# Kernel tuning notes

Measured on AMD Instinct MI355X. Metric: run time of the kernel, lower is better.

## Reference

```python
import jax, jax.numpy as jnp
import numpy as np

N_NODES = 50000
EPS = 1e-7      # GENConv message epsilon
BN_EPS = 1e-5   # BatchNorm1d eps
N_AGGR = 2


def setup_inputs() -> dict:
    key = jax.random.key(0)
    ks = jax.random.split(key, 8)
    C = 64
    E = 800000
    x = jax.random.normal(ks[0], (N_NODES, C), dtype=jnp.float32)
    edge_index = jax.random.randint(ks[1], (2, E), 0, N_NODES, dtype=jnp.int64)
    # per-GENConv MLP params, stacked over the N_AGGR layers
    W1 = jax.random.normal(ks[2], (N_AGGR, C, 2 * C), dtype=jnp.float32) * (1.0 / np.sqrt(C))
    b1 = jnp.zeros((N_AGGR, 2 * C), dtype=jnp.float32)
    gamma = jnp.ones((N_AGGR, 2 * C), dtype=jnp.float32)
    beta = jnp.zeros((N_AGGR, 2 * C), dtype=jnp.float32)
    W2 = jax.random.normal(ks[3], (N_AGGR, 2 * C, C), dtype=jnp.float32) * (1.0 / np.sqrt(2 * C))
    b2 = jnp.zeros((N_AGGR, C), dtype=jnp.float32)
    t = jnp.ones((N_AGGR,), dtype=jnp.float32)  # learnable softmax temperature
    return {"x": x, "edge_index": edge_index, "W1": W1, "b1": b1,
            "gamma": gamma, "beta": beta, "W2": W2, "b2": b2, "t": t}


def _gen_conv(x, src, dst, W1_l, b1_l, gamma_l, beta_l, W2_l, b2_l, t_l):
    # message: relu(x_j) + eps  (edge_attr is None)
    m = jax.nn.relu(x[src]) + EPS                      # [E, C]
    # softmax aggregation over edges grouped by destination node
    logits = m * t_l                                   # [E, C]
    seg_max = jax.ops.segment_max(logits, dst, num_segments=N_NODES)  # [N, C]
    ex = jnp.exp(logits - seg_max[dst])                # [E, C]
    den = jax.ops.segment_sum(ex, dst, num_segments=N_NODES)          # [N, C]
    alpha = ex / (den[dst] + 1e-16)                    # [E, C]
    aggr = jax.ops.segment_sum(m * alpha, dst, num_segments=N_NODES)  # [N, C]
    # residual then MLP: Linear(C,2C) -> BatchNorm1d (train-mode stats) -> ReLU -> Linear(2C,C)
    h = aggr + x
    h = h @ W1_l + b1_l                                # [N, 2C]
    mean = h.mean(axis=0)
    var = h.var(axis=0)                                # biased variance (torch BN)
    h = (h - mean) / jnp.sqrt(var + BN_EPS) * gamma_l + beta_l
    h = jax.nn.relu(h)
    h = h @ W2_l + b2_l                                # [N, C]
    return h


def reference(x, edge_index, W1, b1, gamma, beta, W2, b2, t):
    src = edge_index[0]
    dst = edge_index[1]
    for l in range(N_AGGR):
        x = _gen_conv(x, src, dst, W1[l], b1[l], gamma[l], beta[l], W2[l], b2[l], t[l])
        x = jax.nn.relu(x)
        # dropout in eval mode == identity
    return x
```

## Files before the change

kernel.cpp:

```cpp
#include <hip/hip_runtime.h>
#include <math.h>

#define NN 50000
#define EPSM 1e-7f
#define BN_EPS 1e-5f
#define NBK 391
#define LOG2E 1.44269504088896340736f

#define BN_REP 32
#define MM_REP 8

#if defined(__has_builtin)
#if __has_builtin(__builtin_amdgcn_exp2f)
#define HAVE_EXP2_BUILTIN 1
#endif
#endif
__device__ __forceinline__ float fast_exp2(float v){
#ifdef HAVE_EXP2_BUILTIN
  return __builtin_amdgcn_exp2f(v);
#else
  return exp2f(v);
#endif
}


__global__ __launch_bounds__(256) void bucket_hist_kernel(
    const int* __restrict__ dst, int* __restrict__ bhist, int E,
    unsigned* __restrict__ mm0, float* __restrict__ bn0){
  __shared__ int h[NBK];
  int t = threadIdx.x;
  if (blockIdx.x == 0){
    for (int i = t; i < MM_REP * 128; i += 256)
      mm0[i] = ((i & 127) < 64) ? 0x7F7FFFFFu : 0u;
    for (int i = t; i < BN_REP * 256; i += 256) bn0[i] = 0.f;
  }
  for (int i = t; i < NBK; i += 256) h[i] = 0;
  __syncthreads();
  int e0 = blockIdx.x * 4096;
  int cnt = min(4096, E - e0);
  for (int i = t; i < cnt; i += 256) atomicAdd(&h[dst[e0 + i] >> 7], 1);
  __syncthreads();
  for (int i = t; i < NBK; i += 256) if (h[i]) atomicAdd(&bhist[i], h[i]);
}

__global__ void bucket_scan_kernel(const int* __restrict__ bhist,
                                   int* __restrict__ bbase, int* __restrict__ gcur){
  int lane = threadIdx.x;
  int loc[7]; int s = 0;
#pragma unroll
  for (int k = 0; k < 7; ++k){
    int i = lane * 7 + k;
    int v = (i < NBK) ? bhist[i] : 0;
    loc[k] = s; s += v;
  }
  int sc = s;
#pragma unroll
  for (int o = 1; o < 64; o <<= 1){
    int n = __shfl_up(sc, o);
    if (lane >= o) sc += n;
  }
  int exc = sc - s;
#pragma unroll
  for (int k = 0; k < 7; ++k){
    int i = lane * 7 + k;
    if (i < NBK){ bbase[i] = exc + loc[k]; gcur[i] = exc + loc[k]; }
    else if (i == NBK) bbase[i] = exc + loc[k];
  }
}

__global__ __launch_bounds__(256) void bucket_scatter_kernel(
    const int* __restrict__ src, const int* __restrict__ dst,
    int* __restrict__ gcur, unsigned* __restrict__ packed_g, int E){
  __shared__ int hist[NBK], offs[NBK], gb[NBK], curk[NBK];
  __shared__ unsigned stage[4096];
  __shared__ int gpos[4096];
  int t = threadIdx.x;
  for (int i = t; i < NBK; i += 256) hist[i] = 0;
  __syncthreads();
  int e0 = blockIdx.x * 4096;
  int cnt = min(4096, E - e0);
  unsigned pk[16]; int bk[16];
  int nmine = 0;
  for (int i = t; i < cnt; i += 256){
    int d = dst[e0 + i], s = src[e0 + i];
    pk[nmine] = ((unsigned)d << 16) | (unsigned)s;
    bk[nmine] = d >> 7;
    atomicAdd(&hist[bk[nmine]], 1);
    ++nmine;
  }
  __syncthreads();
  if (t < 64){
    int loc[7]; int s = 0;
#pragma unroll
    for (int k = 0; k < 7; ++k){
      int i = t * 7 + k;
      int v = (i < NBK) ? hist[i] : 0;
      loc[k] = s; s += v;
    }
    int sc = s;
#pragma unroll
    for (int o = 1; o < 64; o <<= 1){
      int n = __shfl_up(sc, o);
      if (t >= o) sc += n;
    }
    int exc = sc - s;
#pragma unroll
    for (int k = 0; k < 7; ++k){
      int i = t * 7 + k;
      if (i < NBK) offs[i] = exc + loc[k];
    }
  }
  __syncthreads();
  for (int i = t; i < NBK; i += 256){
    int h = hist[i];
    gb[i] = h ? atomicAdd(&gcur[i], h) : 0;
    curk[i] = offs[i];
  }
  __syncthreads();
  for (int k = 0; k < nmine; ++k){
    int b = bk[k];
    int p = atomicAdd(&curk[b], 1);
    stage[p] = pk[k];
    gpos[p] = gb[b] + (p - offs[b]);
  }
  __syncthreads();
  for (int j = t; j < cnt; j += 256) packed_g[gpos[j]] = stage[j];
}

__global__ __launch_bounds__(256) void bucket_place_kernel(
    const unsigned* __restrict__ packed_g, const int* __restrict__ bbase,
    int* __restrict__ start_g, int* __restrict__ end_g,
    unsigned short* __restrict__ srcs_g, int N){
  __shared__ int deg[128], off[128], cur[128];
  __shared__ int sstage[4096];
  int b = blockIdx.x, t = threadIdx.x;
  int beg = bbase[b], cnt = bbase[b + 1] - beg;
  if (t < 128) deg[t] = 0;
  __syncthreads();
  for (int j = t; j < cnt; j += 256)
    atomicAdd(&deg[(packed_g[beg + j] >> 16) & 127], 1);
  __syncthreads();
  if (t < 64){
    int i0 = t * 2;
    int v0 = deg[i0], v1 = deg[i0 + 1];
    int s = v0 + v1;
    int sc = s;
#pragma unroll
    for (int o = 1; o < 64; o <<= 1){
      int n = __shfl_up(sc, o);
      if (t >= o) sc += n;
    }
    int exc = sc - s;
    off[i0] = exc; off[i0 + 1] = exc + v0;
  }
  __syncthreads();
  int node0 = b * 128;
  if (t < 128){
    int node = node0 + t;
    if (node < N){
      start_g[node] = beg + off[t];
      end_g[node] = beg + off[t] + deg[t];
    }
    cur[t] = off[t];
  }
  __syncthreads();
  if (cnt <= 4096){
    for (int j = t; j < cnt; j += 256){
      unsigned p = packed_g[beg + j];
      int lp = atomicAdd(&cur[(p >> 16) & 127], 1);
      sstage[lp] = (int)(p & 0xFFFFu);
    }
    __syncthreads();
    for (int j = t; j < cnt; j += 256)
      srcs_g[beg + j] = (unsigned short)sstage[j];
  } else {
    for (int j = t; j < cnt; j += 256){
      unsigned p = packed_g[beg + j];
      int lp = atomicAdd(&cur[(p >> 16) & 127], 1);
      srcs_g[beg + lp] = (unsigned short)(p & 0xFFFFu);
    }
  }
}


__global__ __launch_bounds__(256) void colminmax_kernel(
    const float* __restrict__ x, unsigned* __restrict__ mm,
    unsigned short* __restrict__ mh, int N){
  __shared__ unsigned smn[256], smx[256];
  int c = threadIdx.x & 63;
  int slot = blockIdx.x * 4 + (threadIdx.x >> 6);
  float mx = 0.f, mn = 1e30f;
  for (int r = slot; r < N; r += 256 * 4){
    float m = fmaxf(x[r * 64 + c], 0.f) + EPSM;
    unsigned u = __float_as_uint(m);
    u += 0x7FFFu + ((u >> 16) & 1u);
    unsigned short us = (unsigned short)(u >> 16);
    mh[r * 64 + c] = us;
    float mb = __uint_as_float(((unsigned)us) << 16);
    mx = fmaxf(mx, mb);
    mn = fminf(mn, mb);
  }
  smn[threadIdx.x] = __float_as_uint(mn);
  smx[threadIdx.x] = __float_as_uint(mx);
  __syncthreads();
  if (threadIdx.x < 64){
    int rep = (blockIdx.x & (MM_REP - 1)) * 128;
    unsigned a = smn[c], b = smn[c + 64], d = smn[c + 128], e = smn[c + 192];
    atomicMin(&mm[rep + c], min(min(a, b), min(d, e)));
    a = smx[c]; b = smx[c + 64]; d = smx[c + 128]; e = smx[c + 192];
    atomicMax(&mm[rep + 64 + c], max(max(a, b), max(d, e)));
  }
}


__global__ __launch_bounds__(256) void aggregate_kernel(
    const float* __restrict__ x, const uint2* __restrict__ mh2,
    const int* __restrict__ start, const int* __restrict__ segend,
    const unsigned short* __restrict__ srcs, const float* __restrict__ tptr,
    int layer, const unsigned* __restrict__ mm, float* __restrict__ h0, int N){
  __shared__ float4 Bs4[16];
  int t = threadIdx.x;
  float t2 = tptr[layer] * LOG2E;
  if (t < 64){
    unsigned mn = 0x7F7FFFFFu, mx = 0u;
#pragma unroll
    for (int r = 0; r < MM_REP; ++r){
      mn = min(mn, mm[r * 128 + t]);
      mx = max(mx, mm[r * 128 + 64 + t]);
    }
    ((float*)Bs4)[t] = fmaxf(t2 * __uint_as_float(mx), t2 * __uint_as_float(mn));
  }
  __syncthreads();
  int node = blockIdx.x * 4 + (t >> 6);
  if (node >= N) return;
  int lane = t & 63;
  int slot = lane >> 4, cp = lane & 15;
  float4 B = Bs4[cp];
  int beg = start[node], end = segend[node];
  float d0 = 0.f, d1 = 0.f, d2 = 0.f, d3 = 0.f;
  float n0 = 0.f, n1 = 0.f, n2 = 0.f, n3 = 0.f;
  int e = beg;
  for (; e + 7 < end; e += 8){
    int sA = srcs[e + slot];
    int sB = srcs[e + 4 + slot];
    uint2 uA = mh2[sA * 16 + cp];
    uint2 uB = mh2[sB * 16 + cp];
    float a0 = __uint_as_float(uA.x << 16), a1 = __uint_as_float(uA.x & 0xFFFF0000u);
    float a2 = __uint_as_float(uA.y << 16), a3 = __uint_as_float(uA.y & 0xFFFF0000u);
    float b0 = __uint_as_float(uB.x << 16), b1 = __uint_as_float(uB.x & 0xFFFF0000u);
    float b2 = __uint_as_float(uB.y << 16), b3 = __uint_as_float(uB.y & 0xFFFF0000u);
    float pA0 = fast_exp2(fmaf(a0, t2, -B.x)), pA1 = fast_exp2(fmaf(a1, t2, -B.y));
    float pA2 = fast_exp2(fmaf(a2, t2, -B.z)), pA3 = fast_exp2(fmaf(a3, t2, -B.w));
    float pB0 = fast_exp2(fmaf(b0, t2, -B.x)), pB1 = fast_exp2(fmaf(b1, t2, -B.y));
    float pB2 = fast_exp2(fmaf(b2, t2, -B.z)), pB3 = fast_exp2(fmaf(b3, t2, -B.w));
    d0 += pA0 + pB0; n0 += a0 * pA0 + b0 * pB0;
    d1 += pA1 + pB1; n1 += a1 * pA1 + b1 * pB1;
    d2 += pA2 + pB2; n2 += a2 * pA2 + b2 * pB2;
    d3 += pA3 + pB3; n3 += a3 * pA3 + b3 * pB3;
  }
  for (; e + slot < end; e += 4){
    int s = srcs[e + slot];
    uint2 u = mh2[s * 16 + cp];
    float a0 = __uint_as_float(u.x << 16), a1 = __uint_as_float(u.x & 0xFFFF0000u);
    float a2 = __uint_as_float(u.y << 16), a3 = __uint_as_float(u.y & 0xFFFF0000u);
    float p0 = fast_exp2(fmaf(a0, t2, -B.x)), p1 = fast_exp2(fmaf(a1, t2, -B.y));
    float p2 = fast_exp2(fmaf(a2, t2, -B.z)), p3 = fast_exp2(fmaf(a3, t2, -B.w));
    d0 += p0; n0 += a0 * p0;  d1 += p1; n1 += a1 * p1;
    d2 += p2; n2 += a2 * p2;  d3 += p3; n3 += a3 * p3;
  }
  d0 += __shfl_xor(d0, 16); d1 += __shfl_xor(d1, 16);
  d2 += __shfl_xor(d2, 16); d3 += __shfl_xor(d3, 16);
  n0 += __shfl_xor(n0, 16); n1 += __shfl_xor(n1, 16);
  n2 += __shfl_xor(n2, 16); n3 += __shfl_xor(n3, 16);
  d0 += __shfl_xor(d0, 32); d1 += __shfl_xor(d1, 32);
  d2 += __shfl_xor(d2, 32); d3 += __shfl_xor(d3, 32);
  n0 += __shfl_xor(n0, 32); n1 += __shfl_xor(n1, 32);
  n2 += __shfl_xor(n2, 32); n3 += __shfl_xor(n3, 32);
  if (slot == 0){
    float4 xv = ((const float4*)x)[node * 16 + cp];
    float4 o;
    o.x = n0 / (d0 + 1e-16f) + xv.x;
    o.y = n1 / (d1 + 1e-16f) + xv.y;
    o.z = n2 / (d2 + 1e-16f) + xv.z;
    o.w = n3 / (d3 + 1e-16f) + xv.w;
    ((float4*)h0)[node * 16 + cp] = o;
  }
}


__global__ __launch_bounds__(256) void gemm1_kernel(
    const float* __restrict__ h0, const float* __restrict__ W1,
    const float* __restrict__ b1, float* __restrict__ h1,
    float* __restrict__ bn, int N,
    unsigned* __restrict__ mm_next, float* __restrict__ bn_next){
  __shared__ float a_lds[64 * 68];
  int t = threadIdx.x;
  if (mm_next != 0 && blockIdx.x == 0){
    for (int i = t; i < MM_REP * 128; i += 256)
      mm_next[i] = ((i & 127) < 64) ? 0x7F7FFFFFu : 0u;
    for (int i = t; i < BN_REP * 256; i += 256) bn_next[i] = 0.f;
  }
  int row0 = blockIdx.x * 64;
#pragma unroll
  for (int i = 0; i < 4; ++i){
    int li = t + 256 * i;
    int r = li >> 4, q = li & 15;
    int gr = row0 + r;
    float4 v = make_float4(0.f, 0.f, 0.f, 0.f);
    if (gr < N) v = ((const float4*)h0)[gr * 16 + q];
    *(float4*)&a_lds[r * 68 + q * 4] = v;
  }
  __syncthreads();
  int tc = t & 31, tr = t >> 5;
  float4 bias = ((const float4*)b1)[tc];
  float acc[8][4];
#pragma unroll
  for (int r = 0; r < 8; ++r){
    acc[r][0] = bias.x; acc[r][1] = bias.y; acc[r][2] = bias.z; acc[r][3] = bias.w;
  }
  const float4* wg = (const float4*)W1;
#pragma unroll 2
  for (int k = 0; k < 64; k += 4){
    float4 w0 = wg[(k + 0) * 32 + tc];
    float4 w1 = wg[(k + 1) * 32 + tc];
    float4 w2 = wg[(k + 2) * 32 + tc];
    float4 w3 = wg[(k + 3) * 32 + tc];
#pragma unroll
    for (int r = 0; r < 8; ++r){
      float4 a = *(const float4*)&a_lds[(tr * 8 + r) * 68 + k];
      acc[r][0] += a.x * w0.x + a.y * w1.x + a.z * w2.x + a.w * w3.x;
      acc[r][1] += a.x * w0.y + a.y * w1.y + a.z * w2.y + a.w * w3.y;
      acc[r][2] += a.x * w0.z + a.y * w1.z + a.z * w2.z + a.w * w3.z;
      acc[r][3] += a.x * w0.w + a.y * w1.w + a.z * w2.w + a.w * w3.w;
    }
  }
  float s[4] = {0.f, 0.f, 0.f, 0.f}, s2[4] = {0.f, 0.f, 0.f, 0.f};
#pragma unroll
  for (int r = 0; r < 8; ++r){
    int gr = row0 + tr * 8 + r;
    if (gr < N){
      *(float4*)&h1[gr * 128 + tc * 4] =
          make_float4(acc[r][0], acc[r][1], acc[r][2], acc[r][3]);
#pragma unroll
      for (int j = 0; j < 4; ++j){ s[j] += acc[r][j]; s2[j] += acc[r][j] * acc[r][j]; }
    }
  }
  __syncthreads();
  float* red = a_lds;
  if (t < 256){ red[t] = 0.f; }
  __syncthreads();
#pragma unroll
  for (int j = 0; j < 4; ++j){
    atomicAdd(&red[tc * 4 + j], s[j]);
    atomicAdd(&red[128 + tc * 4 + j], s2[j]);
  }
  __syncthreads();
  if (t < 256) atomicAdd(&bn[(blockIdx.x & (BN_REP - 1)) * 256 + t], red[t]);
}

__global__ __launch_bounds__(256) void gemm2_kernel(
    const float* __restrict__ h1, const float* __restrict__ bn,
    const float* __restrict__ gamma, const float* __restrict__ beta, int layer,
    const float* __restrict__ W2, const float* __restrict__ b2,
    float* __restrict__ xout, int N,
    unsigned* __restrict__ mm_next, unsigned short* __restrict__ mh_next){
  __shared__ float a_lds[64 * 132];
  __shared__ float ss[256];
  __shared__ unsigned smn[64], smx[64];
  int t = threadIdx.x;
  if (t < 128){
    float s = 0.f, s2 = 0.f;
#pragma unroll
    for (int r = 0; r < BN_REP; ++r){
      s  += bn[r * 256 + t];
      s2 += bn[r * 256 + 128 + t];
    }
    float mean = s * (1.f / (float)N);
    float var = s2 * (1.f / (float)N) - mean * mean;
    var = fmaxf(var, 0.f);
    float sc = gamma[layer * 128 + t] / sqrtf(var + BN_EPS);
    ss[t] = sc;
    ss[128 + t] = beta[layer * 128 + t] - mean * sc;
  }
  if (t < 64){ smn[t] = 0x7F7FFFFFu; smx[t] = 0u; }
  __syncthreads();
  int row0 = blockIdx.x * 64;
#pragma unroll
  for (int i = 0; i < 8; ++i){
    int li = t + 256 * i;
    int r = li >> 5, q = li & 31;
    int gr = row0 + r;
    float4 v = make_float4(0.f, 0.f, 0.f, 0.f);
    if (gr < N) v = ((const float4*)h1)[gr * 32 + q];
    float4 sc = *(const float4*)&ss[q * 4];
    float4 sh = *(const float4*)&ss[128 + q * 4];
    v.x = fmaxf(v.x * sc.x + sh.x, 0.f);
    v.y = fmaxf(v.y * sc.y + sh.y, 0.f);
    v.z = fmaxf(v.z * sc.z + sh.z, 0.f);
    v.w = fmaxf(v.w * sc.w + sh.w, 0.f);
    *(float4*)&a_lds[r * 132 + q * 4] = v;
  }
  __syncthreads();
  int tc = t & 15, tr = t >> 4;
  float4 bias = ((const float4*)b2)[tc];
  float acc[4][4];
#pragma unroll
  for (int r = 0; r < 4; ++r){
    acc[r][0] = bias.x; acc[r][1] = bias.y; acc[r][2] = bias.z; acc[r][3] = bias.w;
  }
  const float4* wg = (const float4*)W2;
#pragma unroll 2
  for (int k = 0; k < 128; k += 4){
    float4 w0 = wg[(k + 0) * 16 + tc];
    float4 w1 = wg[(k + 1) * 16 + tc];
    float4 w2 = wg[(k + 2) * 16 + tc];
    float4 w3 = wg[(k + 3) * 16 + tc];
#pragma unroll
    for (int r = 0; r < 4; ++r){
      float4 a = *(const float4*)&a_lds[(tr * 4 + r) * 132 + k];
      acc[r][0] += a.x * w0.x + a.y * w1.x + a.z * w2.x + a.w * w3.x;
      acc[r][1] += a.x * w0.y + a.y * w1.y + a.z * w2.y + a.w * w3.y;
      acc[r][2] += a.x * w0.z + a.y * w1.z + a.z * w2.z + a.w * w3.z;
      acc[r][3] += a.x * w0.w + a.y * w1.w + a.z * w2.w + a.w * w3.w;
    }
  }
  unsigned mnv[4] = {0x7F7FFFFFu, 0x7F7FFFFFu, 0x7F7FFFFFu, 0x7F7FFFFFu};
  unsigned mxv[4] = {0u, 0u, 0u, 0u};
#pragma unroll
  for (int r = 0; r < 4; ++r){
    int gr = row0 + tr * 4 + r;
    if (gr < N){
      float o0 = fmaxf(acc[r][0], 0.f), o1 = fmaxf(acc[r][1], 0.f);
      float o2 = fmaxf(acc[r][2], 0.f), o3 = fmaxf(acc[r][3], 0.f);
      *(float4*)&xout[gr * 64 + tc * 4] = make_float4(o0, o1, o2, o3);
      if (mh_next != 0){
        unsigned us[4];
        float ov[4] = {o0, o1, o2, o3};
#pragma unroll
        for (int j = 0; j < 4; ++j){
          unsigned u = __float_as_uint(ov[j] + EPSM);
          u += 0x7FFFu + ((u >> 16) & 1u);
          us[j] = u >> 16;
          unsigned fb = us[j] << 16;
          mnv[j] = min(mnv[j], fb);
          mxv[j] = max(mxv[j], fb);
        }
        ((uint2*)mh_next)[gr * 16 + tc] =
            make_uint2(us[0] | (us[1] << 16), us[2] | (us[3] << 16));
      }
    }
  }
  if (mh_next != 0){
    __syncthreads();
#pragma unroll
    for (int j = 0; j < 4; ++j){
      atomicMin(&smn[tc * 4 + j], mnv[j]);
      atomicMax(&smx[tc * 4 + j], mxv[j]);
    }
    __syncthreads();
    if (t < 64){
      int rep = (blockIdx.x & (MM_REP - 1)) * 128;
      atomicMin(&mm_next[rep + t], smn[t]);
      atomicMax(&mm_next[rep + 64 + t], smx[t]);
    }
  }
}

extern "C" void kernel_launch(void* const* d_in, const int* in_sizes, int n_in,
                              void* d_out, int out_size, void* d_ws, size_t ws_size,
                              hipStream_t stream) {
  const float* x0    = (const float*)d_in[0];
  const int*   ei    = (const int*)d_in[1];
  const float* W1    = (const float*)d_in[2];
  const float* b1    = (const float*)d_in[3];
  const float* gamma = (const float*)d_in[4];
  const float* beta  = (const float*)d_in[5];
  const float* W2    = (const float*)d_in[6];
  const float* b2    = (const float*)d_in[7];
  const float* tptr  = (const float*)d_in[8];

  const int N = NN;
  const int E = in_sizes[1] / 2;
  const int* src = ei;
  const int* dst = ei + E;

  float* ws  = (float*)d_ws;
  float* h0  = ws;
  float* h1  = h0 + N * 64;
  float* bn0 = h1 + N * 128;
  float* bn1 = bn0 + BN_REP * 256;
  unsigned* mm0 = (unsigned*)(bn1 + BN_REP * 256);
  unsigned* mm1 = mm0 + MM_REP * 128;
  unsigned short* mh = (unsigned short*)(mm1 + MM_REP * 128);
  int* bhist = (int*)(mh + N * 64);
  int* bbase = bhist + NBK;
  int* gcur  = bbase + NBK + 1;
  int* start = gcur + NBK;
  int* segend = start + N;
  unsigned* packed = (unsigned*)(segend + N);
  unsigned short* srcs = (unsigned short*)(packed + E);

  float* out = (float*)d_out;

  const int row_blocks = (N + 63) / 64;
  const int chunk_blocks = (E + 4095) / 4096;
  const int agg_blocks = (N + 3) / 4;

  hipMemsetAsync(bhist, 0, NBK * sizeof(int), stream);
  bucket_hist_kernel<<<chunk_blocks, 256, 0, stream>>>(dst, bhist, E, mm0, bn0);
  bucket_scan_kernel<<<1, 64, 0, stream>>>(bhist, bbase, gcur);
  bucket_scatter_kernel<<<chunk_blocks, 256, 0, stream>>>(src, dst, gcur, packed, E);
  bucket_place_kernel<<<NBK, 256, 0, stream>>>(packed, bbase, start, segend, srcs, N);

  colminmax_kernel<<<256, 256, 0, stream>>>(x0, mm0, mh, N);
  aggregate_kernel<<<agg_blocks, 256, 0, stream>>>(x0, (const uint2*)mh, start,
                                                   segend, srcs, tptr, 0, mm0, h0, N);
  gemm1_kernel<<<row_blocks, 256, 0, stream>>>(h0, W1, b1, h1, bn0, N, mm1, bn1);
  gemm2_kernel<<<row_blocks, 256, 0, stream>>>(h1, bn0, gamma, beta, 0, W2, b2,
                                               out, N, mm1, mh);
  aggregate_kernel<<<agg_blocks, 256, 0, stream>>>(out, (const uint2*)mh, start,
                                                   segend, srcs, tptr, 1, mm1, h0, N);
  gemm1_kernel<<<row_blocks, 256, 0, stream>>>(h0, W1 + 8192, b1 + 128, h1, bn1, N,
                                               (unsigned*)0, (float*)0);
  gemm2_kernel<<<row_blocks, 256, 0, stream>>>(h1, bn1, gamma, beta, 1, W2 + 8192,
                                               b2 + 64, out, N,
                                               (unsigned*)0, (unsigned short*)0);
}
```

Before: 300.9 us.

## Derive BatchNorm stats from input second moments and fuse both GEMMs

Instead of materializing the 128-wide hidden activation h1 to compute BatchNorm statistics, a moments kernel computes the 64x64 Gram matrix and column sums of the GEMM input. A single-block stats kernel then projects them through W1 to get the mean and variance of h1. A fused MLP kernel recomputes GEMM1, applies BN+ReLU in registers/LDS, and runs GEMM2, which removes the write and re-read of the 50000x128 h1 buffer. This adds a serial single-block reduction over 196 partials, redundant GEMM1 work, and a possible loss of precision from computing variance via E[x^2]-mean^2 on the projected moments.

New measurement: 433.6 us. 1.44x slower.

```diff
diff --git a/kernel.cpp b/kernel.cpp
--- a/kernel.cpp
+++ b/kernel.cpp
@@ -6,9 +6,9 @@
 #define BN_EPS 1e-5f
 #define NBK 391
 #define LOG2E 1.44269504088896340736f
-
-#define BN_REP 32
 #define MM_REP 8
+#define MOM_BLOCKS 196
+#define MOM_STRIDE 4352
 
 #if defined(__has_builtin)
 #if __has_builtin(__builtin_amdgcn_exp2f)
@@ -26,13 +26,12 @@
 
 __global__ __launch_bounds__(256) void bucket_hist_kernel(
     const int* __restrict__ dst, int* __restrict__ bhist, int E,
-    unsigned* __restrict__ mm0, float* __restrict__ bn0){
+    unsigned* __restrict__ mm0){
   __shared__ int h[NBK];
   int t = threadIdx.x;
   if (blockIdx.x == 0){
-    for (int i = t; i < MM_REP * 128; i += 256)
+    for (int i = t; i < 2 * MM_REP * 128; i += 256)
       mm0[i] = ((i & 127) < 64) ? 0x7F7FFFFFu : 0u;
-    for (int i = t; i < BN_REP * 256; i += 256) bn0[i] = 0.f;
   }
   for (int i = t; i < NBK; i += 256) h[i] = 0;
   __syncthreads();
@@ -288,18 +287,126 @@
 }
 
 
-__global__ __launch_bounds__(256) void gemm1_kernel(
+__global__ __launch_bounds__(256) void moments_kernel(
+    const float* __restrict__ h0, float* __restrict__ part){
+  __shared__ float rs[16][64];
+  int t = threadIdx.x;
+  float m[4][4];
+#pragma unroll
+  for (int a = 0; a < 4; ++a)
+#pragma unroll
+    for (int b = 0; b < 4; ++b) m[a][b] = 0.f;
+  float cs = 0.f;
+  int i0 = (t >> 4) * 4, j0 = (t & 15) * 4;
+  int lr = t >> 4, lq = t & 15;
+  int ch = t & 63, r0 = t >> 6;
+  int base = blockIdx.x * 256;
+  for (int c = 0; c < 16; ++c){
+    __syncthreads();
+    int gr = base + c * 16 + lr;
+    float4 v = make_float4(0.f, 0.f, 0.f, 0.f);
+    if (gr < NN) v = ((const float4*)h0)[gr * 16 + lq];
+    *(float4*)&rs[lr][lq * 4] = v;
+    __syncthreads();
+#pragma unroll
+    for (int rr = 0; rr < 16; ++rr){
+      float4 av = *(const float4*)&rs[rr][i0];
+      float4 bv = *(const float4*)&rs[rr][j0];
+      m[0][0] += av.x * bv.x; m[0][1] += av.x * bv.y;
+      m[0][2] += av.x * bv.z; m[0][3] += av.x * bv.w;
+      m[1][0] += av.y * bv.x; m[1][1] += av.y * bv.y;
+      m[1][2] += av.y * bv.z; m[1][3] += av.y * bv.w;
+      m[2][0] += av.z * bv.x; m[2][1] += av.z * bv.y;
+      m[2][2] += av.z * bv.z; m[2][3] += av.z * bv.w;
+      m[3][0] += av.w * bv.x; m[3][1] += av.w * bv.y;
+      m[3][2] += av.w * bv.z; m[3][3] += av.w * bv.w;
+    }
+    cs += rs[r0][ch] + rs[r0 + 4][ch] + rs[r0 + 8][ch] + rs[r0 + 12][ch];
+  }
+  float* pb = part + blockIdx.x * MOM_STRIDE;
+#pragma unroll
+  for (int a = 0; a < 4; ++a)
+    *(float4*)&pb[(i0 + a) * 64 + j0] = make_float4(m[a][0], m[a][1], m[a][2], m[a][3]);
+  pb[4096 + t] = cs;
+}
+
+
+__global__ __launch_bounds__(256) void stats_kernel(
+    const float* __restrict__ part, const float* __restrict__ W1,
+    const float* __restrict__ b1, const float* __restrict__ gamma,
+    const float* __restrict__ beta, int layer, float* __restrict__ ssg){
+  __shared__ float M[64][64];
+  __shared__ float s[64];
+  __shared__ float w[64][128];
+  __shared__ float qp[2][128], swp[2][128];
+  int t = threadIdx.x;
+  int i0 = (t >> 4) * 4, j0 = (t & 15) * 4;
+  float a0x=0,a0y=0,a0z=0,a0w=0, a1x=0,a1y=0,a1z=0,a1w=0;
+  float a2x=0,a2y=0,a2z=0,a2w=0, a3x=0,a3y=0,a3z=0,a3w=0;
+  for (int p = 0; p < MOM_BLOCKS; ++p){
+    const float* pb = part + p * MOM_STRIDE;
+    float4 v0 = *(const float4*)&pb[(i0 + 0) * 64 + j0];
+    float4 v1 = *(const float4*)&pb[(i0 + 1) * 64 + j0];
+    float4 v2 = *(const float4*)&pb[(i0 + 2) * 64 + j0];
+    float4 v3 = *(const float4*)&pb[(i0 + 3) * 64 + j0];
+    a0x += v0.x; a0y += v0.y; a0z += v0.z; a0w += v0.w;
+    a1x += v1.x; a1y += v1.y; a1z += v1.z; a1w += v1.w;
+    a2x += v2.x; a2y += v2.y; a2z += v2.z; a2w += v2.w;
+    a3x += v3.x; a3y += v3.y; a3z += v3.z; a3w += v3.w;
+  }
+  *(float4*)&M[i0 + 0][j0] = make_float4(a0x, a0y, a0z, a0w);
+  *(float4*)&M[i0 + 1][j0] = make_float4(a1x, a1y, a1z, a1w);
+  *(float4*)&M[i0 + 2][j0] = make_float4(a2x, a2y, a2z, a2w);
+  *(float4*)&M[i0 + 3][j0] = make_float4(a3x, a3y, a3z, a3w);
+  if (t < 64){
+    float v = 0.f;
+    for (int p = 0; p < MOM_BLOCKS; ++p){
+      const float* pc = part + p * MOM_STRIDE + 4096;
+      v += (pc[t] + pc[64 + t]) + (pc[128 + t] + pc[192 + t]);
+    }
+    s[t] = v;
+  }
+  const float4* wg = (const float4*)W1;
+  for (int i = t; i < 2048; i += 256) ((float4*)w)[i] = wg[i];
+  __syncthreads();
+  int j = t & 127, half = t >> 7;
+  float q = 0.f, sw = 0.f;
+  for (int i = half * 32; i < half * 32 + 32; ++i){
+    float dot = 0.f;
+#pragma unroll 8
+    for (int k = 0; k < 64; ++k) dot += M[i][k] * w[k][j];
+    q += w[i][j] * dot;
+  }
+  for (int k = half * 32; k < half * 32 + 32; ++k) sw += s[k] * w[k][j];
+  qp[half][j] = q; swp[half][j] = sw;
+  __syncthreads();
+  if (t < 128){
+    float qt = qp[0][t] + qp[1][t];
+    float swt = swp[0][t] + swp[1][t];
+    float bj = b1[t];
+    float invN = 1.f / (float)NN;
+    float mean = swt * invN + bj;
+    float e2 = (qt + 2.f * bj * swt) * invN + bj * bj;
+    float var = fmaxf(e2 - mean * mean, 0.f);
+    float sc = gamma[layer * 128 + t] / sqrtf(var + BN_EPS);
+    ssg[t] = sc;
+    ssg[128 + t] = beta[layer * 128 + t] - mean * sc;
+  }
+}
+
+
+__global__ __launch_bounds__(256) void fused_mlp_kernel(
     const float* __restrict__ h0, const float* __restrict__ W1,
-    const float* __restrict__ b1, float* __restrict__ h1,
-    float* __restrict__ bn, int N,
-    unsigned* __restrict__ mm_next, float* __restrict__ bn_next){
-  __shared__ float a_lds[64 * 68];
+    const float* __restrict__ b1, const float* __restrict__ ssg,
+    const float* __restrict__ W2, const float* __restrict__ b2,
+    float* __restrict__ xout, int N,
+    unsigned* __restrict__ mm_next, unsigned short* __restrict__ mh_next){
+  __shared__ float lds[64 * 132];
+  __shared__ float ss[256];
+  __shared__ unsigned smn[64], smx[64];
   int t = threadIdx.x;
-  if (mm_next != 0 && blockIdx.x == 0){
-    for (int i = t; i < MM_REP * 128; i += 256)
-      mm_next[i] = ((i & 127) < 64) ? 0x7F7FFFFFu : 0u;
-    for (int i = t; i < BN_REP * 256; i += 256) bn_next[i] = 0.f;
-  }
+  ss[t] = ssg[t];
+  if (t < 64){ smn[t] = 0x7F7FFFFFu; smx[t] = 0u; }
   int row0 = blockIdx.x * 64;
 #pragma unroll
   for (int i = 0; i < 4; ++i){
@@ -308,131 +415,79 @@
     int gr = row0 + r;
     float4 v = make_float4(0.f, 0.f, 0.f, 0.f);
     if (gr < N) v = ((const float4*)h0)[gr * 16 + q];
-    *(float4*)&a_lds[r * 68 + q * 4] = v;
+    *(float4*)&lds[r * 68 + q * 4] = v;
   }
   __syncthreads();
   int tc = t & 31, tr = t >> 5;
-  float4 bias = ((const float4*)b1)[tc];
-  float acc[8][4];
+  float4 bias1 = ((const float4*)b1)[tc];
+  float acc1[8][4];
 #pragma unroll
   for (int r = 0; r < 8; ++r){
-    acc[r][0] = bias.x; acc[r][1] = bias.y; acc[r][2] = bias.z; acc[r][3] = bias.w;
-  }
-  const float4* wg = (const float4*)W1;
+    acc1[r][0] = bias1.x; acc1[r][1] = bias1.y;
+    acc1[r][2] = bias1.z; acc1[r][3] = bias1.w;
+  }
+  const float4* wg1 = (const float4*)W1;
 #pragma unroll 2
   for (int k = 0; k < 64; k += 4){
-    float4 w0 = wg[(k + 0) * 32 + tc];
-    float4 w1 = wg[(k + 1) * 32 + tc];
-    float4 w2 = wg[(k + 2) * 32 + tc];
-    float4 w3 = wg[(k + 3) * 32 + tc];
+    float4 w0 = wg1[(k + 0) * 32 + tc];
+    float4 w1 = wg1[(k + 1) * 32 + tc];
+    float4 w2 = wg1[(k + 2) * 32 + tc];
+    float4 w3 = wg1[(k + 3) * 32 + tc];
 #pragma unroll
     for (int r = 0; r < 8; ++r){
-      float4 a = *(const float4*)&a_lds[(tr * 8 + r) * 68 + k];
-      acc[r][0] += a.x * w0.x + a.y * w1.x + a.z * w2.x + a.w * w3.x;
-      acc[r][1] += a.x * w0.y + a.y * w1.y + a.z * w2.y + a.w * w3.y;
-      acc[r][2] += a.x * w0.z + a.y * w1.z + a.z * w2.z + a.w * w3.z;
-      acc[r][3] += a.x * w0.w + a.y * w1.w + a.z * w2.w + a.w * w3.w;
-    }
-  }
-  float s[4] = {0.f, 0.f, 0.f, 0.f}, s2[4] = {0.f, 0.f, 0.f, 0.f};
+      float4 a = *(const float4*)&lds[(tr * 8 + r) * 68 + k];
+      acc1[r][0] += a.x * w0.x + a.y * w1.x + a.z * w2.x + a.w * w3.x;
+      acc1[r][1] += a.x * w0.y + a.y * w1.y + a.z * w2.y + a.w * w3.y;
+      acc1[r][2] += a.x * w0.z + a.y * w1.z + a.z * w2.z + a.w * w3.z;
+      acc1[r][3] += a.x * w0.w + a.y * w1.w + a.z * w2.w + a.w * w3.w;
+    }
+  }
+  __syncthreads();
+  float4 sc4 = *(const float4*)&ss[tc * 4];
+  float4 sh4 = *(const float4*)&ss[128 + tc * 4];
 #pragma unroll
   for (int r = 0; r < 8; ++r){
-    int gr = row0 + tr * 8 + r;
-    if (gr < N){
-      *(float4*)&h1[gr * 128 + tc * 4] =
-          make_float4(acc[r][0], acc[r][1], acc[r][2], acc[r][3]);
-#pragma unroll
-      for (int j = 0; j < 4; ++j){ s[j] += acc[r][j]; s2[j] += acc[r][j] * acc[r][j]; }
-    }
-  }
-  __syncthreads();
-  float* red = a_lds;
-  if (t < 256){ red[t] = 0.f; }
-  __syncthreads();
-#pragma unroll
-  for (int j = 0; j < 4; ++j){
-    atomicAdd(&red[tc * 4 + j], s[j]);
-    atomicAdd(&red[128 + tc * 4 + j], s2[j]);
-  }
-  __syncthreads();
-  if (t < 256) atomicAdd(&bn[(blockIdx.x & (BN_REP - 1)) * 256 + t], red[t]);
-}
-
-__global__ __launch_bounds__(256) void gemm2_kernel(
-    const float* __restrict__ h1, const float* __restrict__ bn,
-    const float* __restrict__ gamma, const float* __restrict__ beta, int layer,
-    const float* __restrict__ W2, const float* __restrict__ b2,
-    float* __restrict__ xout, int N,
-    unsigned* __restrict__ mm_next, unsigned short* __restrict__ mh_next){
-  __shared__ float a_lds[64 * 132];
-  __shared__ float ss[256];
-  __shared__ unsigned smn[64], smx[64];
-  int t = threadIdx.x;
-  if (t < 128){
-    float s = 0.f, s2 = 0.f;
-#pragma unroll
-    for (int r = 0; r < BN_REP; ++r){
-      s  += bn[r * 256 + t];
-      s2 += bn[r * 256 + 128 + t];
-    }
-    float mean = s * (1.f / (float)N);
-    float var = s2 * (1.f / (float)N) - mean * mean;
-    var = fmaxf(var, 0.f);
-    float sc = gamma[layer * 128 + t] / sqrtf(var + BN_EPS);
-    ss[t] = sc;
-    ss[128 + t] = beta[layer * 128 + t] - mean * sc;
-  }
-  if (t < 64){ smn[t] = 0x7F7FFFFFu; smx[t] = 0u; }
-  __syncthreads();
-  int row0 = blockIdx.x * 64;
-#pragma unroll
-  for (int i = 0; i < 8; ++i){
-    int li = t + 256 * i;
-    int r = li >> 5, q = li & 31;
-    int gr = row0 + r;
-    float4 v = make_float4(0.f, 0.f, 0.f, 0.f);
-    if (gr < N) v = ((const float4*)h1)[gr * 32 + q];
-    float4 sc = *(const float4*)&ss[q * 4];
-    float4 sh = *(const float4*)&ss[128 + q * 4];
-    v.x = fmaxf(v.x * sc.x + sh.x, 0.f);
-    v.y = fmaxf(v.y * sc.y + sh.y, 0.f);
-    v.z = fmaxf(v.z * sc.z + sh.z, 0.f);
-    v.w = fmaxf(v.w * sc.w + sh.w, 0.f);
-    *(float4*)&a_lds[r * 132 + q * 4] = v;
-  }
-  __syncthreads();
-  int tc = t & 15, tr = t >> 4;
-  float4 bias = ((const float4*)b2)[tc];
-  float acc[4][4];
+    float4 o;
+    o.x = fmaxf(acc1[r][0] * sc4.x + sh4.x, 0.f);
+    o.y = fmaxf(acc1[r][1] * sc4.y + sh4.y, 0.f);
+    o.z = fmaxf(acc1[r][2] * sc4.z + sh4.z, 0.f);
+    o.w = fmaxf(acc1[r][3] * sc4.w + sh4.w, 0.f);
+    *(float4*)&lds[(tr * 8 + r) * 132 + tc * 4] = o;
+  }
+  __syncthreads();
+  int tc2 = t & 15, tr2 = t >> 4;
+  float4 bias2 = ((const float4*)b2)[tc2];
+  float acc2[4][4];
 #pragma unroll
   for (int r = 0; r < 4; ++r){
-    acc[r][0] = bias.x; acc[r][1] = bias.y; acc[r][2] = bias.z; acc[r][3] = bias.w;
-  }
-  const float4* wg = (const float4*)W2;
+    acc2[r][0] = bias2.x; acc2[r][1] = bias2.y;
+    acc2[r][2] = bias2.z; acc2[r][3] = bias2.w;
+  }
+  const float4* wg2 = (const float4*)W2;
 #pragma unroll 2
   for (int k = 0; k < 128; k += 4){
-    float4 w0 = wg[(k + 0) * 16 + tc];
-    float4 w1 = wg[(k + 1) * 16 + tc];
-    float4 w2 = wg[(k + 2) * 16 + tc];
-    float4 w3 = wg[(k + 3) * 16 + tc];
+    float4 w0 = wg2[(k + 0) * 16 + tc2];
+    float4 w1 = wg2[(k + 1) * 16 + tc2];
+    float4 w2 = wg2[(k + 2) * 16 + tc2];
+    float4 w3 = wg2[(k + 3) * 16 + tc2];
 #pragma unroll
     for (int r = 0; r < 4; ++r){
-      float4 a = *(const float4*)&a_lds[(tr * 4 + r) * 132 + k];
-      acc[r][0] += a.x * w0.x + a.y * w1.x + a.z * w2.x + a.w * w3.x;
-      acc[r][1] += a.x * w0.y + a.y * w1.y + a.z * w2.y + a.w * w3.y;
-      acc[r][2] += a.x * w0.z + a.y * w1.z + a.z * w2.z + a.w * w3.z;
-      acc[r][3] += a.x * w0.w + a.y * w1.w + a.z * w2.w + a.w * w3.w;
+      float4 a = *(const float4*)&lds[(tr2 * 4 + r) * 132 + k];
+      acc2[r][0] += a.x * w0.x + a.y * w1.x + a.z * w2.x + a.w * w3.x;
+      acc2[r][1] += a.x * w0.y + a.y * w1.y + a.z * w2.y + a.w * w3.y;
+      acc2[r][2] += a.x * w0.z + a.y * w1.z + a.z * w2.z + a.w * w3.z;
+      acc2[r][3] += a.x * w0.w + a.y * w1.w + a.z * w2.w + a.w * w3.w;
     }
   }
   unsigned mnv[4] = {0x7F7FFFFFu, 0x7F7FFFFFu, 0x7F7FFFFFu, 0x7F7FFFFFu};
   unsigned mxv[4] = {0u, 0u, 0u, 0u};
 #pragma unroll
   for (int r = 0; r < 4; ++r){
-    int gr = row0 + tr * 4 + r;
+    int gr = row0 + tr2 * 4 + r;
     if (gr < N){
-      float o0 = fmaxf(acc[r][0], 0.f), o1 = fmaxf(acc[r][1], 0.f);
-      float o2 = fmaxf(acc[r][2], 0.f), o3 = fmaxf(acc[r][3], 0.f);
-      *(float4*)&xout[gr * 64 + tc * 4] = make_float4(o0, o1, o2, o3);
+      float o0 = fmaxf(acc2[r][0], 0.f), o1 = fmaxf(acc2[r][1], 0.f);
+      float o2 = fmaxf(acc2[r][2], 0.f), o3 = fmaxf(acc2[r][3], 0.f);
+      *(float4*)&xout[gr * 64 + tc2 * 4] = make_float4(o0, o1, o2, o3);
       if (mh_next != 0){
         unsigned us[4];
         float ov[4] = {o0, o1, o2, o3};
@@ -445,7 +500,7 @@
           mnv[j] = min(mnv[j], fb);
           mxv[j] = max(mxv[j], fb);
         }
-        ((uint2*)mh_next)[gr * 16 + tc] =
+        ((uint2*)mh_next)[gr * 16 + tc2] =
             make_uint2(us[0] | (us[1] << 16), us[2] | (us[3] << 16));
       }
     }
@@ -454,8 +509,8 @@
     __syncthreads();
 #pragma unroll
     for (int j = 0; j < 4; ++j){
-      atomicMin(&smn[tc * 4 + j], mnv[j]);
-      atomicMax(&smx[tc * 4 + j], mxv[j]);
+      atomicMin(&smn[tc2 * 4 + j], mnv[j]);
+      atomicMax(&smx[tc2 * 4 + j], mxv[j]);
     }
     __syncthreads();
     if (t < 64){
@@ -486,12 +541,12 @@
 
   float* ws  = (float*)d_ws;
   float* h0  = ws;
-  float* h1  = h0 + N * 64;
-  float* bn0 = h1 + N * 128;
-  float* bn1 = bn0 + BN_REP * 256;
-  unsigned* mm0 = (unsigned*)(bn1 + BN_REP * 256);
+  unsigned* mm0 = (unsigned*)(h0 + N * 64);
   unsigned* mm1 = mm0 + MM_REP * 128;
-  unsigned short* mh = (unsigned short*)(mm1 + MM_REP * 128);
+  float* ss0 = (float*)(mm1 + MM_REP * 128);
+  float* ss1 = ss0 + 256;
+  float* part = ss1 + 256;
+  unsigned short* mh = (unsigned short*)(part + MOM_BLOCKS * MOM_STRIDE);
   int* bhist = (int*)(mh + N * 64);
   int* bbase = bhist + NBK;
   int* gcur  = bbase + NBK + 1;
@@ -507,7 +562,7 @@
   const int agg_blocks = (N + 3) / 4;
 
   hipMemsetAsync(bhist, 0, NBK * sizeof(int), stream);
-  bucket_hist_kernel<<<chunk_blocks, 256, 0, stream>>>(dst, bhist, E, mm0, bn0);
+  bucket_hist_kernel<<<chunk_blocks, 256, 0, stream>>>(dst, bhist, E, mm0);
   bucket_scan_kernel<<<1, 64, 0, stream>>>(bhist, bbase, gcur);
   bucket_scatter_kernel<<<chunk_blocks, 256, 0, stream>>>(src, dst, gcur, packed, E);
   bucket_place_kernel<<<NBK, 256, 0, stream>>>(packed, bbase, start, segend, srcs, N);
@@ -515,14 +570,15 @@
   colminmax_kernel<<<256, 256, 0, stream>>>(x0, mm0, mh, N);
   aggregate_kernel<<<agg_blocks, 256, 0, stream>>>(x0, (const uint2*)mh, start,
                                                    segend, srcs, tptr, 0, mm0, h0, N);
-  gemm1_kernel<<<row_blocks, 256, 0, stream>>>(h0, W1, b1, h1, bn0, N, mm1, bn1);
-  gemm2_kernel<<<row_blocks, 256, 0, stream>>>(h1, bn0, gamma, beta, 0, W2, b2,
-                                               out, N, mm1, mh);
+  moments_kernel<<<MOM_BLOCKS, 256, 0, stream>>>(h0, part);
+  stats_kernel<<<1, 256, 0, stream>>>(part, W1, b1, gamma, beta, 0, ss0);
+  fused_mlp_kernel<<<row_blocks, 256, 0, stream>>>(h0, W1, b1, ss0, W2, b2,
+                                                   out, N, mm1, mh);
   aggregate_kernel<<<agg_blocks, 256, 0, stream>>>(out, (const uint2*)mh, start,
                                                    segend, srcs, tptr, 1, mm1, h0, N);
-  gemm1_kernel<<<row_blocks, 256, 0, stream>>>(h0, W1 + 8192, b1 + 128, h1, bn1, N,
-                                               (unsigned*)0, (float*)0);
-  gemm2_kernel<<<row_blocks, 256, 0, stream>>>(h1, bn1, gamma, beta, 1, W2 + 8192,
-                                               b2 + 64, out, N,
-                                               (unsigned*)0, (unsigned short*)0);
-}
+  moments_kernel<<<MOM_BLOCKS, 256, 0, stream>>>(h0, part);
+  stats_kernel<<<1, 256, 0, stream>>>(part, W1 + 8192, b1 + 128, gamma, beta, 1, ss1);
+  fused_mlp_kernel<<<row_blocks, 256, 0, stream>>>(h0, W1 + 8192, b1 + 128, ss1,
+                                                   W2 + 8192, b2 + 64, out, N,
+                                                   (unsigned*)0, (unsigned short*)0);
+}
```
